# Kernel tuning notes

Hardware: AMD Instinct MI355X
Metric: run time of the kernel (lower is better)

Reference implementation:

```python
import jax, jax.numpy as jnp
import numpy as np

N_PATCH, N_Z, K, BS = 16, 128, 10, 1024
D = N_PATCH * N_Z


def setup_inputs() -> dict:
    key = jax.random.key(0)
    k1, k2, k3, k4 = jax.random.split(key, 4)
    z = jax.random.normal(k1, (BS, D), dtype=jnp.float32)
    m = jax.random.normal(k2, (K, D), dtype=jnp.float32)
    L = jax.random.normal(k3, (K, D, D), dtype=jnp.float32)
    components = jax.random.randint(k4, (BS,), 0, K, dtype=jnp.int64)
    return {"z": z, "m": m, "L": L, "components": components}


def reference(z, m, L, components):
    # samps[k] = m[k] + z @ L[k].T   -> (K, BS, D)
    samps = jnp.einsum('bd,ked->kbe', z, L) + m[:, None, :]
    # one-hot mask-and-sum over components == gather selected expert per sample
    x = samps[components, jnp.arange(z.shape[0])]  # (BS, D)
    return x.reshape(-1, N_PATCH, N_Z)
```

## Files before the change

kernel.cpp:

```cpp
#include <hip/hip_runtime.h>
#include <hip/hip_bf16.h>


#define DDIM  2048
#define BSAMP 1024
#define KCOMP 10
#define MPAD  160
#define NT    64
#define BK    32
#define ZREG  10240
#define STAGE 18432

typedef __attribute__((ext_vector_type(8))) short bf16x8;
typedef __attribute__((ext_vector_type(4))) float f32x4;

__device__ __forceinline__ void async16(void* lds, const void* g) {
    __builtin_amdgcn_global_load_lds(
        (const __attribute__((address_space(1))) void*)g,
        (__attribute__((address_space(3))) void*)lds, 16, 0, 0);
}
__device__ __forceinline__ short bfs(float x) {
    __hip_bfloat16 h = __float2bfloat16(x);
    return *reinterpret_cast<short*>(&h);
}
__device__ __forceinline__ bf16x8 packB(const char* rowb, int o0, int o1) {
    f32x4 x = *(const f32x4*)(rowb + o0);
    f32x4 y = *(const f32x4*)(rowb + o1);
    bf16x8 r;
#pragma unroll
    for (int i = 0; i < 4; ++i) { r[i] = bfs(x[i]); r[4 + i] = bfs(y[i]); }
    return r;
}

__global__ void build_map(const int* __restrict__ comp,
                          int* __restrict__ rowmap,
                          int* __restrict__ counts) {
    __shared__ int sc[KCOMP];
    const int t = threadIdx.x;
    if (t < KCOMP) sc[t] = 0;
    __syncthreads();
    const int c = comp[t];
    const int r = atomicAdd(&sc[c], 1);
    if (r < MPAD) rowmap[c * MPAD + r] = t;
    __syncthreads();
    if (t < KCOMP) counts[t] = sc[t];
}

__global__ void zconv(const float* __restrict__ z, short* __restrict__ zb) {
    const int i = (blockIdx.x * 256 + threadIdx.x) * 8;
    f32x4 a = *(const f32x4*)(z + i);
    f32x4 b = *(const f32x4*)(z + i + 4);
    bf16x8 o;
#pragma unroll
    for (int j = 0; j < 4; ++j) { o[j] = bfs(a[j]); o[4 + j] = bfs(b[j]); }
    *(bf16x8*)(zb + i) = o;
}

__device__ __forceinline__ int swz(int r) { return (r & 3) ^ ((r >> 2) & 3); }

__global__ __launch_bounds__(256, 4)
void gmm_bf16z(const short* __restrict__ zb,
               const float* __restrict__ mvec,
               const float* __restrict__ Lmat,
               const int* __restrict__ rowmap,
               const int* __restrict__ counts,
               float* __restrict__ out) {
    __shared__ __attribute__((aligned(16))) char smem[2 * STAGE];
    const int t = threadIdx.x, lane = t & 63;
    const int w = t >> 6, mh = w >> 1, nh = w & 1;
    const int k = blockIdx.y, n0 = blockIdx.x * NT;
    const float* Lk = Lmat + (size_t)k * DDIM * DDIM;
    const int cnt = counts[k];

    const int zq = t >> 2, zcs = t & 3;
    const int zr1 = 64 + zq, zr2 = 128 + zq;
    const int rmB = k * MPAD;
    const int rm0 = rowmap[rmB + zq] & (BSAMP - 1);
    const int rm1 = rowmap[rmB + zr1] & (BSAMP - 1);
    const int rm2 = rowmap[rmB + ((zr2 < MPAD) ? zr2 : 0)] & (BSAMP - 1);
    const short* zp0 = zb + (size_t)rm0 * DDIM + (zcs ^ swz(zq)) * 8;
    const short* zp1 = zb + (size_t)rm1 * DDIM + (zcs ^ swz(zr1)) * 8;
    const short* zp2 = zb + (size_t)rm2 * DDIM + (zcs ^ swz(zr2)) * 8;
    const int lcs = t & 7;
    const int lr2 = (t >= 128) ? ((t - 128) >> 3) : 0;
    const int lr3 = 16 + (t >> 3);
    const int lr4 = 48 + (t >> 3);
    const float* lp2 = Lk + (size_t)(n0 + lr2) * DDIM + (lcs ^ (lr2 & 7)) * 4;
    const float* lp3 = Lk + (size_t)(n0 + lr3) * DDIM + (lcs ^ (lr3 & 7)) * 4;
    const float* lp4 = Lk + (size_t)(n0 + (lr4 & 63)) * DDIM + (lcs ^ (lr4 & 7)) * 4;
    const int ub  = (t & ~63) << 4;
    const int ubh = ((t - 128) & ~63) << 4;
    const bool lowHalf = (t < 128);
    const bool st1 = (cnt > 64), st2 = (cnt > 128);

    auto stage = [&](int buf, int it) {
        char* lb = smem + buf * STAGE;
        const int d = it * BK;
        async16(lb + ub, zp0 + d);
        if (st1) async16(lb + 4096 + ub, zp1 + d);
        if (lowHalf) {
            if (st2) async16(lb + 8192 + ub, zp2 + d);
            async16(lb + ZREG + 6144 + ub, lp4 + d);
        } else {
            async16(lb + ZREG + ubh, lp2 + d);
        }
        async16(lb + ZREG + 2048 + ub, lp3 + d);
    };

    f32x4 acc[5][2];
#pragma unroll
    for (int mt = 0; mt < 5; ++mt)
#pragma unroll
        for (int nt = 0; nt < 2; ++nt) acc[mt][nt] = (f32x4){0.f, 0.f, 0.f, 0.f};

    stage(0, 0);
    __syncthreads();

    const int fr = lane & 15, g = lane >> 4;
    const int szA   = (fr & 3) ^ ((fr >> 2) & 3);
    const int aoff  = ((g ^ szA) & 3) * 16;
    const int boff0 = (((g * 2)     ^ (fr & 7)) & 7) * 16;
    const int boff1 = (((g * 2 + 1) ^ (fr & 7)) & 7) * 16;
    const int rb0 = (nh * 32 + fr) * 128, rb1 = (nh * 32 + 16 + fr) * 128;
    const int raB = (mh * 80 + fr) * 64;

    for (int it = 0; it < DDIM / BK; ++it) {
        if (it + 1 < DDIM / BK) stage((it + 1) & 1, it + 1);
        const char* lb = smem + (it & 1) * STAGE;
        const char* Lb = lb + ZREG;
        bf16x8 b0 = packB(Lb + rb0, boff0, boff1);
        bf16x8 b1 = packB(Lb + rb1, boff0, boff1);
#pragma unroll
        for (int mt = 0; mt < 5; ++mt) {
            bf16x8 a = *(const bf16x8*)(lb + raB + mt * 16 * 64 + aoff);
            acc[mt][0] = __builtin_amdgcn_mfma_f32_16x16x32_bf16(a, b0, acc[mt][0], 0, 0, 0);
            acc[mt][1] = __builtin_amdgcn_mfma_f32_16x16x32_bf16(a, b1, acc[mt][1], 0, 0, 0);
        }
        __syncthreads();
    }

    const int rquad = (lane >> 4) * 4;
#pragma unroll
    for (int nt = 0; nt < 2; ++nt) {
        const int e = n0 + nh * 32 + nt * 16 + fr;
        const float mu = mvec[k * DDIM + e];
#pragma unroll
        for (int mt = 0; mt < 5; ++mt) {
            const int sb = mh * 80 + mt * 16 + rquad;
#pragma unroll
            for (int r = 0; r < 4; ++r) {
                const int slot = sb + r;
                if (slot < cnt) {
                    const int b = rowmap[rmB + slot];
                    out[(size_t)b * DDIM + e] = acc[mt][nt][r] + mu;
                }
            }
        }
    }
}

__device__ __forceinline__ bf16x8 frag8(const char* base, int o0, int o1) {
    f32x4 x = *(const f32x4*)(base + o0);
    f32x4 y = *(const f32x4*)(base + o1);
    bf16x8 r;
#pragma unroll
    for (int i = 0; i < 4; ++i) { r[i] = bfs(x[i]); r[4 + i] = bfs(y[i]); }
    return r;
}
__global__ __launch_bounds__(256, 2)
void gmm_f32z(const float* __restrict__ z, const float* __restrict__ mvec,
              const float* __restrict__ Lmat, const int* __restrict__ rowmap,
              const int* __restrict__ counts, float* __restrict__ out) {
    __shared__ __attribute__((aligned(16))) char smem[2 * 28672];
    const int t = threadIdx.x, lane = t & 63, w = t >> 6;
    const int mh = w >> 1, nh = w & 1;
    const int k = blockIdx.y, n0 = blockIdx.x * NT;
    const float* Lk = Lmat + (size_t)k * DDIM * DDIM;
    const int rq = t >> 3;
    const int scol = ((t & 7) ^ (rq & 7)) * 4;
    int rm[5];
#pragma unroll
    for (int j = 0; j < 5; ++j)
        rm[j] = rowmap[k * MPAD + j * 32 + rq] & (BSAMP - 1);
    const unsigned ub = (unsigned)(t & ~63) * 16;
    auto stage = [&](int buf, int it) {
        char* lb = smem + buf * 28672;
        const int d0 = it * 32 + scol;
#pragma unroll
        for (int j = 0; j < 5; ++j)
            async16(lb + j * 4096 + ub, z + (size_t)rm[j] * DDIM + d0);
        async16(lb + 20480 + ub,        Lk + (size_t)(n0 + rq) * DDIM + d0);
        async16(lb + 20480 + 4096 + ub, Lk + (size_t)(n0 + 32 + rq) * DDIM + d0);
    };
    f32x4 acc[5][2];
#pragma unroll
    for (int mt = 0; mt < 5; ++mt)
#pragma unroll
        for (int nt = 0; nt < 2; ++nt) acc[mt][nt] = (f32x4){0.f, 0.f, 0.f, 0.f};
    stage(0, 0);
    __syncthreads();
    const int fr = lane & 15, g0 = (lane >> 4) * 2;
    for (int it = 0; it < DDIM / 32; ++it) {
        if (it + 1 < DDIM / 32) stage((it + 1) & 1, it + 1);
        const char* lb = smem + (it & 1) * 28672;
        const int rb0 = nh * 32 + fr, rb1 = rb0 + 16;
        bf16x8 b0 = frag8(lb + 20480, rb0 * 128 + ((g0 ^ rb0) & 7) * 16,
                          rb0 * 128 + (((g0 + 1) ^ rb0) & 7) * 16);
        bf16x8 b1 = frag8(lb + 20480, rb1 * 128 + ((g0 ^ rb1) & 7) * 16,
                          rb1 * 128 + (((g0 + 1) ^ rb1) & 7) * 16);
#pragma unroll
        for (int mt = 0; mt < 5; ++mt) {
            const int ra = mh * 80 + mt * 16 + fr;
            bf16x8 a = frag8(lb, ra * 128 + ((g0 ^ ra) & 7) * 16,
                             ra * 128 + (((g0 + 1) ^ ra) & 7) * 16);
            acc[mt][0] = __builtin_amdgcn_mfma_f32_16x16x32_bf16(a, b0, acc[mt][0], 0, 0, 0);
            acc[mt][1] = __builtin_amdgcn_mfma_f32_16x16x32_bf16(a, b1, acc[mt][1], 0, 0, 0);
        }
        __syncthreads();
    }
    const int cnt = counts[k], rquad = (lane >> 4) * 4;
#pragma unroll
    for (int nt = 0; nt < 2; ++nt) {
        const int e = n0 + nh * 32 + nt * 16 + fr;
        const float mu = mvec[k * DDIM + e];
#pragma unroll
        for (int mt = 0; mt < 5; ++mt) {
            const int sb = mh * 80 + mt * 16 + rquad;
#pragma unroll
            for (int r = 0; r < 4; ++r) {
                const int slot = sb + r;
                if (slot < cnt)
                    out[(size_t)rowmap[k * MPAD + slot] * DDIM + e] = acc[mt][nt][r] + mu;
            }
        }
    }
}

extern "C" void kernel_launch(void* const* d_in, const int* in_sizes, int n_in,
                              void* d_out, int out_size, void* d_ws, size_t ws_size,
                              hipStream_t stream) {
    const float* z    = (const float*)d_in[0];
    const float* mvec = (const float*)d_in[1];
    const float* Lmat = (const float*)d_in[2];
    const int* comp   = (const int*)d_in[3];
    float* out        = (float*)d_out;

    int* rowmap = (int*)d_ws;
    int* counts = rowmap + KCOMP * MPAD;
    build_map<<<1, BSAMP, 0, stream>>>(comp, rowmap, counts);

    const size_t need = 8192 + (size_t)BSAMP * DDIM * 2;
    if (ws_size >= need) {
        short* zbuf = (short*)((char*)d_ws + 8192);
        zconv<<<BSAMP * DDIM / (256 * 8), 256, 0, stream>>>(z, zbuf);
        gmm_bf16z<<<dim3(DDIM / NT, KCOMP), 256, 0, stream>>>(
            zbuf, mvec, Lmat, rowmap, counts, out);
    } else {
        gmm_f32z<<<dim3(DDIM / NT, KCOMP), 256, 0, stream>>>(
            z, mvec, Lmat, rowmap, counts, out);
    }
}
```

Measured before the change: 274.8 us.

## Split the D reduction four ways with partial buffers and a separate reduce kernel

Splits the inner dimension of the per-component GEMM into four chunks across a third grid dimension, writing fp32 partial sums to workspace. A new reduce kernel sums the partials and adds the mean vector per sample. MFMA work on M tiles beyond the component's row count is also skipped. This raises the block count to fill the GPU better, at the cost of extra global traffic for the partial buffers and an extra launch, and it requires a larger workspace.

```diff
diff --git a/kernel.cpp b/kernel.cpp
--- a/kernel.cpp
+++ b/kernel.cpp
@@ -8,6 +8,8 @@
 #define MPAD  160
 #define NT    64
 #define BK    32
+#define SPLITK 4
+#define DCHUNK (DDIM / SPLITK)
 #define ZREG  10240
 #define STAGE 18432
 
@@ -59,16 +61,16 @@
 __device__ __forceinline__ int swz(int r) { return (r & 3) ^ ((r >> 2) & 3); }
 
 __global__ __launch_bounds__(256, 4)
-void gmm_bf16z(const short* __restrict__ zb,
-               const float* __restrict__ mvec,
-               const float* __restrict__ Lmat,
-               const int* __restrict__ rowmap,
-               const int* __restrict__ counts,
-               float* __restrict__ out) {
+void gmm_splitk(const short* __restrict__ zb,
+                const float* __restrict__ Lmat,
+                const int* __restrict__ rowmap,
+                const int* __restrict__ counts,
+                float* __restrict__ partial) {
     __shared__ __attribute__((aligned(16))) char smem[2 * STAGE];
     const int t = threadIdx.x, lane = t & 63;
     const int w = t >> 6, mh = w >> 1, nh = w & 1;
     const int k = blockIdx.y, n0 = blockIdx.x * NT;
+    const int kc = blockIdx.z, dbase = kc * DCHUNK;
     const float* Lk = Lmat + (size_t)k * DDIM * DDIM;
     const int cnt = counts[k];
 
@@ -78,16 +80,16 @@
     const int rm0 = rowmap[rmB + zq] & (BSAMP - 1);
     const int rm1 = rowmap[rmB + zr1] & (BSAMP - 1);
     const int rm2 = rowmap[rmB + ((zr2 < MPAD) ? zr2 : 0)] & (BSAMP - 1);
-    const short* zp0 = zb + (size_t)rm0 * DDIM + (zcs ^ swz(zq)) * 8;
-    const short* zp1 = zb + (size_t)rm1 * DDIM + (zcs ^ swz(zr1)) * 8;
-    const short* zp2 = zb + (size_t)rm2 * DDIM + (zcs ^ swz(zr2)) * 8;
+    const short* zp0 = zb + (size_t)rm0 * DDIM + dbase + (zcs ^ swz(zq)) * 8;
+    const short* zp1 = zb + (size_t)rm1 * DDIM + dbase + (zcs ^ swz(zr1)) * 8;
+    const short* zp2 = zb + (size_t)rm2 * DDIM + dbase + (zcs ^ swz(zr2)) * 8;
     const int lcs = t & 7;
     const int lr2 = (t >= 128) ? ((t - 128) >> 3) : 0;
     const int lr3 = 16 + (t >> 3);
     const int lr4 = 48 + (t >> 3);
-    const float* lp2 = Lk + (size_t)(n0 + lr2) * DDIM + (lcs ^ (lr2 & 7)) * 4;
-    const float* lp3 = Lk + (size_t)(n0 + lr3) * DDIM + (lcs ^ (lr3 & 7)) * 4;
-    const float* lp4 = Lk + (size_t)(n0 + (lr4 & 63)) * DDIM + (lcs ^ (lr4 & 7)) * 4;
+    const float* lp2 = Lk + (size_t)(n0 + lr2) * DDIM + dbase + (lcs ^ (lr2 & 7)) * 4;
+    const float* lp3 = Lk + (size_t)(n0 + lr3) * DDIM + dbase + (lcs ^ (lr3 & 7)) * 4;
+    const float* lp4 = Lk + (size_t)(n0 + (lr4 & 63)) * DDIM + dbase + (lcs ^ (lr4 & 7)) * 4;
     const int ub  = (t & ~63) << 4;
     const int ubh = ((t - 128) & ~63) << 4;
     const bool lowHalf = (t < 128);
@@ -124,26 +126,28 @@
     const int rb0 = (nh * 32 + fr) * 128, rb1 = (nh * 32 + 16 + fr) * 128;
     const int raB = (mh * 80 + fr) * 64;
 
-    for (int it = 0; it < DDIM / BK; ++it) {
-        if (it + 1 < DDIM / BK) stage((it + 1) & 1, it + 1);
+    for (int it = 0; it < DCHUNK / BK; ++it) {
+        if (it + 1 < DCHUNK / BK) stage((it + 1) & 1, it + 1);
         const char* lb = smem + (it & 1) * STAGE;
         const char* Lb = lb + ZREG;
         bf16x8 b0 = packB(Lb + rb0, boff0, boff1);
         bf16x8 b1 = packB(Lb + rb1, boff0, boff1);
 #pragma unroll
         for (int mt = 0; mt < 5; ++mt) {
-            bf16x8 a = *(const bf16x8*)(lb + raB + mt * 16 * 64 + aoff);
-            acc[mt][0] = __builtin_amdgcn_mfma_f32_16x16x32_bf16(a, b0, acc[mt][0], 0, 0, 0);
-            acc[mt][1] = __builtin_amdgcn_mfma_f32_16x16x32_bf16(a, b1, acc[mt][1], 0, 0, 0);
+            if (mh * 80 + mt * 16 < cnt) {
+                bf16x8 a = *(const bf16x8*)(lb + raB + mt * 16 * 64 + aoff);
+                acc[mt][0] = __builtin_amdgcn_mfma_f32_16x16x32_bf16(a, b0, acc[mt][0], 0, 0, 0);
+                acc[mt][1] = __builtin_amdgcn_mfma_f32_16x16x32_bf16(a, b1, acc[mt][1], 0, 0, 0);
+            }
         }
         __syncthreads();
     }
 
+    float* pk = partial + (size_t)kc * BSAMP * DDIM;
     const int rquad = (lane >> 4) * 4;
 #pragma unroll
     for (int nt = 0; nt < 2; ++nt) {
         const int e = n0 + nh * 32 + nt * 16 + fr;
-        const float mu = mvec[k * DDIM + e];
 #pragma unroll
         for (int mt = 0; mt < 5; ++mt) {
             const int sb = mh * 80 + mt * 16 + rquad;
@@ -152,11 +156,31 @@
                 const int slot = sb + r;
                 if (slot < cnt) {
                     const int b = rowmap[rmB + slot];
-                    out[(size_t)b * DDIM + e] = acc[mt][nt][r] + mu;
+                    pk[(size_t)b * DDIM + e] = acc[mt][nt][r];
                 }
             }
         }
     }
+}
+
+__global__ void reduce_out(const float* __restrict__ partial,
+                           const float* __restrict__ mvec,
+                           const int* __restrict__ comp,
+                           float* __restrict__ out) {
+    const int b = blockIdx.x;
+    const int c = comp[b];
+    const int e = threadIdx.x * 8;
+    const float* pb = partial + (size_t)b * DDIM + e;
+    f32x4 s0 = *(const f32x4*)(mvec + (size_t)c * DDIM + e);
+    f32x4 s1 = *(const f32x4*)(mvec + (size_t)c * DDIM + e + 4);
+#pragma unroll
+    for (int kc = 0; kc < SPLITK; ++kc) {
+        const float* p = pb + (size_t)kc * BSAMP * DDIM;
+        s0 += *(const f32x4*)(p);
+        s1 += *(const f32x4*)(p + 4);
+    }
+    *(f32x4*)(out + (size_t)b * DDIM + e)     = s0;
+    *(f32x4*)(out + (size_t)b * DDIM + e + 4) = s1;
 }
 
 __device__ __forceinline__ bf16x8 frag8(const char* base, int o0, int o1) {
@@ -249,12 +273,18 @@
     int* counts = rowmap + KCOMP * MPAD;
     build_map<<<1, BSAMP, 0, stream>>>(comp, rowmap, counts);
 
-    const size_t need = 8192 + (size_t)BSAMP * DDIM * 2;
-    if (ws_size >= need) {
-        short* zbuf = (short*)((char*)d_ws + 8192);
+    const size_t zb_off = 8192;
+    const size_t zb_sz  = (size_t)BSAMP * DDIM * 2;
+    const size_t p_off  = zb_off + zb_sz;
+    const size_t p_sz   = (size_t)SPLITK * BSAMP * DDIM * 4;
+
+    if (ws_size >= p_off + p_sz) {
+        short* zbuf    = (short*)((char*)d_ws + zb_off);
+        float* partial = (float*)((char*)d_ws + p_off);
         zconv<<<BSAMP * DDIM / (256 * 8), 256, 0, stream>>>(z, zbuf);
-        gmm_bf16z<<<dim3(DDIM / NT, KCOMP), 256, 0, stream>>>(
-            zbuf, mvec, Lmat, rowmap, counts, out);
+        gmm_splitk<<<dim3(DDIM / NT, KCOMP, SPLITK), 256, 0, stream>>>(
+            zbuf, Lmat, rowmap, counts, partial);
+        reduce_out<<<BSAMP, DDIM / 8, 0, stream>>>(partial, mvec, comp, out);
     } else {
         gmm_f32z<<<dim3(DDIM / NT, KCOMP), 256, 0, stream>>>(
             z, mvec, Lmat, rowmap, counts, out);
```

Result: slower. 293.8 us (+6.9%).
